# Performance work log

Hardware: AMD Instinct MI355X
Metric: run time of the kernel (lower is better)

The kernel has to match this reference:

```python
import jax, jax.numpy as jnp
import numpy as np

HIDDEN = 64
NUM_HEADS = 2
HEAD_DIM = HIDDEN // NUM_HEADS  # 32


def setup_inputs() -> dict:
    key = jax.random.key(0)
    ks = jax.random.split(key, 10)
    B, L = 8, 2048
    s = 1.0 / np.sqrt(HIDDEN)
    return {
        "hidden_states": jax.random.normal(ks[0], (B, L, HIDDEN), dtype=jnp.float32),
        "qx": jax.random.normal(ks[1], (B, L, HIDDEN), dtype=jnp.float32),
        "Wq": jax.random.uniform(ks[2], (HIDDEN, HIDDEN), jnp.float32, -s, s),
        "bq": jax.random.uniform(ks[3], (HIDDEN,), jnp.float32, -s, s),
        "Wk": jax.random.uniform(ks[4], (HIDDEN, HIDDEN), jnp.float32, -s, s),
        "bk": jax.random.uniform(ks[5], (HIDDEN,), jnp.float32, -s, s),
        "Wv": jax.random.uniform(ks[6], (HIDDEN, HIDDEN), jnp.float32, -s, s),
        "bv": jax.random.uniform(ks[7], (HIDDEN,), jnp.float32, -s, s),
        "Wo": jax.random.uniform(ks[8], (HIDDEN, HIDDEN), jnp.float32, -s, s),
        "bo": jax.random.uniform(ks[9], (HIDDEN,), jnp.float32, -s, s),
    }


def _split_heads(x):
    # [B, L, HIDDEN] -> [B, H, L, HEAD_DIM]
    B, L, _ = x.shape
    return x.reshape(B, L, NUM_HEADS, HEAD_DIM).transpose(0, 2, 1, 3)


def reference(hidden_states, qx, Wq, bq, Wk, bk, Wv, bv, Wo, bo):
    # NOTE: faithful to original - query AND value come from qx, key from hidden_states.
    q = _split_heads(qx @ Wq.T + bq)              # [B, H, Lq, D]
    k = _split_heads(hidden_states @ Wk.T + bk)   # [B, H, Lk, D]
    v = _split_heads(qx @ Wv.T + bv)              # [B, H, Lq, D]
    scores = jnp.einsum("bhqd,bhkd->bhqk", q, k) / np.sqrt(HEAD_DIM).astype(np.float32)
    probs = jax.nn.softmax(scores, axis=-1)       # [B, H, Lq, Lk]
    ctx = jnp.einsum("bhqk,bhkd->bhqd", probs, v)
    B, H, L, D = ctx.shape
    ctx = ctx.transpose(0, 2, 1, 3).reshape(B, L, H * D)
    out = ctx @ Wo.T + bo
    return out, probs
```

## Files before the change

kernel.cpp:

```cpp
#include <hip/hip_runtime.h>
#include <math.h>

#define NB 8
#define SEQ 2048
#define HID 64
#define HDIM 32
#define ROWS (NB * SEQ)
#define OUT_ELEMS (ROWS * HID)
#define QSCALE 0.25503486f

typedef __attribute__((ext_vector_type(8))) short bf16x8;
typedef __attribute__((ext_vector_type(4))) float f32x4;
typedef __attribute__((ext_vector_type(4))) uint u32x4;

__device__ __forceinline__ ushort f2bf(float f) {
    uint u = __builtin_bit_cast(uint, f);
    u += 0x7FFFu + ((u >> 16) & 1u);
    return (ushort)(u >> 16);
}
__device__ __forceinline__ float bf2f(ushort h) {
    uint u = ((uint)h) << 16;
    return __builtin_bit_cast(float, u);
}
__device__ __forceinline__ uint cvt_pk_bf16(float lo, float hi) {
    uint r;
    asm("v_cvt_pk_bf16_f32 %0, %1, %2" : "=v"(r) : "v"(lo), "v"(hi));
    return r;
}

__global__ __launch_bounds__(256, 1)
void qkv_proj_kernel(const float* __restrict__ hs, const float* __restrict__ qx,
                     const float* __restrict__ Wq, const float* __restrict__ bq,
                     const float* __restrict__ Wk, const float* __restrict__ bk,
                     const float* __restrict__ Wv, const float* __restrict__ bv,
                     ushort* __restrict__ q_hi, ushort* __restrict__ q_lo,
                     ushort* __restrict__ k_hi, ushort* __restrict__ vt_hi)
{
    __shared__ __align__(16) float xq_lds[64][64];
    __shared__ __align__(16) float xh_lds[64][64];
    __shared__ float vbuf[64][65];

    const int t  = threadIdx.x;
    const int r0 = blockIdx.x * 64;
    const int b  = r0 >> 11;

#pragma unroll
    for (int u = 0; u < 4; ++u) {
        const int idx = t + 256 * u;
        const int rr = idx >> 4, kk = (idx & 15) * 4;
        *(float4*)&xq_lds[rr][kk] = *(const float4*)(qx + (size_t)(r0 + rr) * HID + kk);
        *(float4*)&xh_lds[rr][kk] = *(const float4*)(hs + (size_t)(r0 + rr) * HID + kk);
    }
    __syncthreads();

    const int c = t & 63, w = t >> 6;
    const int rw = w * 16;
    const int h = c >> 5, d = c & 31;
    const size_t obase = ((size_t)((b * 2 + h) * SEQ) + (r0 & 2047) + rw) * 32 + d;

    {
        float4 wr[16];
#pragma unroll
        for (int i = 0; i < 16; ++i) wr[i] = *(const float4*)(Wq + c * 64 + 4 * i);
        const float bc = bq[c];
        f32x4 acc[16];
#pragma unroll
        for (int r = 0; r < 16; ++r) acc[r] = (f32x4){0.f, 0.f, 0.f, 0.f};
#pragma unroll
        for (int k4 = 0; k4 < 16; ++k4) {
#pragma unroll
            for (int r = 0; r < 16; ++r) {
                const float4 x4 = *(const float4*)&xq_lds[rw + r][k4 * 4];
                acc[r][0] += x4.x * wr[k4].x; acc[r][1] += x4.y * wr[k4].y;
                acc[r][2] += x4.z * wr[k4].z; acc[r][3] += x4.w * wr[k4].w;
            }
        }
#pragma unroll
        for (int r = 0; r < 16; ++r) {
            const float v = (acc[r][0] + acc[r][1] + acc[r][2] + acc[r][3] + bc) * QSCALE;
            const ushort hv = f2bf(v);
            q_hi[obase + (size_t)r * 32] = hv;
            q_lo[obase + (size_t)r * 32] = f2bf(v - bf2f(hv));
        }
    }
    {
        float4 wr[16];
#pragma unroll
        for (int i = 0; i < 16; ++i) wr[i] = *(const float4*)(Wk + c * 64 + 4 * i);
        const float bc = bk[c];
        f32x4 acc[16];
#pragma unroll
        for (int r = 0; r < 16; ++r) acc[r] = (f32x4){0.f, 0.f, 0.f, 0.f};
#pragma unroll
        for (int k4 = 0; k4 < 16; ++k4) {
#pragma unroll
            for (int r = 0; r < 16; ++r) {
                const float4 x4 = *(const float4*)&xh_lds[rw + r][k4 * 4];
                acc[r][0] += x4.x * wr[k4].x; acc[r][1] += x4.y * wr[k4].y;
                acc[r][2] += x4.z * wr[k4].z; acc[r][3] += x4.w * wr[k4].w;
            }
        }
#pragma unroll
        for (int r = 0; r < 16; ++r) {
            const float v = acc[r][0] + acc[r][1] + acc[r][2] + acc[r][3] + bc;
            k_hi[obase + (size_t)r * 32] = f2bf(v);
        }
    }
    {
        float4 wr[16];
#pragma unroll
        for (int i = 0; i < 16; ++i) wr[i] = *(const float4*)(Wv + c * 64 + 4 * i);
        const float bc = bv[c];
        f32x4 acc[16];
#pragma unroll
        for (int r = 0; r < 16; ++r) acc[r] = (f32x4){0.f, 0.f, 0.f, 0.f};
#pragma unroll
        for (int k4 = 0; k4 < 16; ++k4) {
#pragma unroll
            for (int r = 0; r < 16; ++r) {
                const float4 x4 = *(const float4*)&xq_lds[rw + r][k4 * 4];
                acc[r][0] += x4.x * wr[k4].x; acc[r][1] += x4.y * wr[k4].y;
                acc[r][2] += x4.z * wr[k4].z; acc[r][3] += x4.w * wr[k4].w;
            }
        }
#pragma unroll
        for (int r = 0; r < 16; ++r)
            vbuf[rw + r][c] = acc[r][0] + acc[r][1] + acc[r][2] + acc[r][3] + bc;
    }
    __syncthreads();

#pragma unroll
    for (int g = 0; g < 2; ++g) {
        const int row8 = (g * 4 + w) * 8;
        bf16x8 hi8;
#pragma unroll
        for (int e = 0; e < 8; ++e) hi8[e] = (short)f2bf(vbuf[row8 + e][c]);
        const size_t vo = ((size_t)((b * 2 + h) * 32) + d) * SEQ + (r0 & 2047) + row8;
        *reinterpret_cast<bf16x8*>(vt_hi + vo) = hi8;
    }
}

__global__ __launch_bounds__(256, 4)
void attn_kernel(const ushort* __restrict__ q_hi, const ushort* __restrict__ q_lo,
                 const ushort* __restrict__ k_hi, const ushort* __restrict__ vt_hi,
                 float* __restrict__ d_out)
{
    __shared__ float z_buf[4][32];
    __shared__ __align__(16) float ctx_buf[4][32][32];
    __shared__ __align__(16) float pstage[4][512];

    const int bid   = blockIdx.x;
    const int swz   = (bid & 7) * 128 + (bid >> 3);
    const int slice = swz >> 6;
    const int qb    = swz & 63;
    const int bb = slice >> 1, hh = slice & 1;
    const int q0 = qb * 32;

    const int tid  = threadIdx.x;
    const int w    = tid >> 6, lane = tid & 63;
    const int lg   = lane >> 4, li = lane & 15;
    const int cq0  = w * 512;

    bf16x8 aqh[2], aql[2];
#pragma unroll
    for (int rt = 0; rt < 2; ++rt) {
        const size_t qoff = ((size_t)slice * SEQ + q0 + rt * 16 + li) * 32 + lg * 8;
        aqh[rt] = *reinterpret_cast<const bf16x8*>(q_hi + qoff);
        aql[rt] = *reinterpret_cast<const bf16x8*>(q_lo + qoff);
    }

    const size_t kbase = (size_t)slice * SEQ * 32;
    const size_t vbase = (size_t)slice * 32 * SEQ;

    auto Kfrag = [&](int j16) {
        return *reinterpret_cast<const bf16x8*>(
            k_hi + kbase + (size_t)(cq0 + j16 * 16 + li) * 32 + lg * 8);
    };
    auto Vfrag = [&](int c2, int dt) {
        return *reinterpret_cast<const bf16x8*>(
            vt_hi + vbase + (size_t)(dt * 16 + li) * SEQ + cq0 + c2 * 32 + lg * 8);
    };

    float zacc[8];
#pragma unroll
    for (int i = 0; i < 8; ++i) zacc[i] = 0.f;
    {
        bf16x8 bh = Kfrag(0);
#pragma unroll 2
        for (int ct = 0; ct < 32; ++ct) {
            const bf16x8 bn = Kfrag(ct < 31 ? ct + 1 : 31);
#pragma unroll
            for (int rt = 0; rt < 2; ++rt) {
                f32x4 acc = {0.f, 0.f, 0.f, 0.f};
                acc = __builtin_amdgcn_mfma_f32_16x16x32_bf16(aqh[rt], bh, acc, 0, 0, 0);
                acc = __builtin_amdgcn_mfma_f32_16x16x32_bf16(aql[rt], bh, acc, 0, 0, 0);
#pragma unroll
                for (int r = 0; r < 4; ++r)
                    zacc[rt * 4 + r] += __builtin_amdgcn_exp2f(acc[r]);
            }
            bh = bn;
        }
    }
#pragma unroll
    for (int m = 1; m < 16; m <<= 1) {
#pragma unroll
        for (int i = 0; i < 8; ++i) zacc[i] += __shfl_xor(zacc[i], m, 64);
    }
    if (li == 0) {
#pragma unroll
        for (int rt = 0; rt < 2; ++rt)
#pragma unroll
            for (int r = 0; r < 4; ++r)
                z_buf[w][rt * 16 + lg * 4 + r] = zacc[rt * 4 + r];
    }
    __syncthreads();
    float rcpz[8];
#pragma unroll
    for (int rt = 0; rt < 2; ++rt)
#pragma unroll
        for (int r = 0; r < 4; ++r) {
            const int row = rt * 16 + lg * 4 + r;
            rcpz[rt * 4 + r] = 1.0f / (z_buf[0][row] + z_buf[1][row] +
                                       z_buf[2][row] + z_buf[3][row]);
        }

    f32x4 pacc[2][2];
#pragma unroll
    for (int rt = 0; rt < 2; ++rt)
#pragma unroll
        for (int dt = 0; dt < 2; ++dt) pacc[rt][dt] = (f32x4){0.f, 0.f, 0.f, 0.f};

    float* probs = d_out + OUT_ELEMS + ((size_t)slice * SEQ + q0) * SEQ;
    float* ps = &pstage[w][0];

    bf16x8 k0 = Kfrag(0), k1 = Kfrag(1);
    bf16x8 v0 = Vfrag(0, 0), v1 = Vfrag(0, 1);

#pragma unroll 1
    for (int c2 = 0; c2 < 16; ++c2) {
        const int cn = (c2 < 15) ? c2 + 1 : 15;
        const bf16x8 k0n = Kfrag(2 * cn),     k1n = Kfrag(2 * cn + 1);
        const bf16x8 v0n = Vfrag(cn, 0),      v1n = Vfrag(cn, 1);

        bf16x8 ap[2];
#pragma unroll
        for (int rt = 0; rt < 2; ++rt) {
            f32x4 a0 = {0.f, 0.f, 0.f, 0.f}, a1 = {0.f, 0.f, 0.f, 0.f};
            a0 = __builtin_amdgcn_mfma_f32_16x16x32_bf16(aqh[rt], k0, a0, 0, 0, 0);
            a0 = __builtin_amdgcn_mfma_f32_16x16x32_bf16(aql[rt], k0, a0, 0, 0, 0);
            a1 = __builtin_amdgcn_mfma_f32_16x16x32_bf16(aqh[rt], k1, a1, 0, 0, 0);
            a1 = __builtin_amdgcn_mfma_f32_16x16x32_bf16(aql[rt], k1, a1, 0, 0, 0);
#pragma unroll
            for (int r = 0; r < 4; ++r) {
                const int row = lg * 4 + r;
                const float p0 = __builtin_amdgcn_exp2f(a0[r]) * rcpz[rt * 4 + r];
                const float p1 = __builtin_amdgcn_exp2f(a1[r]) * rcpz[rt * 4 + r];
                ps[row * 32 + (li ^ (lg << 3))]        = p0;
                ps[row * 32 + ((16 + li) ^ (lg << 3))] = p1;
            }
#pragma unroll
            for (int u = 0; u < 2; ++u) {
                const int fid = lane + 64 * u;
                const int row = fid >> 3, c4 = fid & 7;
                const int pcb = (c4 * 4) ^ (((row >> 2) & 3) << 3);
                const f32x4 pv = *reinterpret_cast<const f32x4*>(&ps[row * 32 + pcb]);
                __builtin_nontemporal_store(pv, reinterpret_cast<f32x4*>(
                    probs + (size_t)(rt * 16 + row) * SEQ + cq0 + c2 * 32 + c4 * 4));
            }
            const int abase = li * 32 + ((lg ^ ((li >> 2) & 3)) << 3);
            const f32x4 pa = *reinterpret_cast<const f32x4*>(&ps[abase]);
            const f32x4 pb = *reinterpret_cast<const f32x4*>(&ps[abase + 4]);
            u32x4 pk;
            pk[0] = cvt_pk_bf16(pa[0], pa[1]); pk[1] = cvt_pk_bf16(pa[2], pa[3]);
            pk[2] = cvt_pk_bf16(pb[0], pb[1]); pk[3] = cvt_pk_bf16(pb[2], pb[3]);
            ap[rt] = __builtin_bit_cast(bf16x8, pk);
        }
#pragma unroll
        for (int rt = 0; rt < 2; ++rt) {
            pacc[rt][0] = __builtin_amdgcn_mfma_f32_16x16x32_bf16(ap[rt], v0, pacc[rt][0], 0, 0, 0);
            pacc[rt][1] = __builtin_amdgcn_mfma_f32_16x16x32_bf16(ap[rt], v1, pacc[rt][1], 0, 0, 0);
        }
        k0 = k0n; k1 = k1n; v0 = v0n; v1 = v1n;
    }

#pragma unroll
    for (int rt = 0; rt < 2; ++rt)
#pragma unroll
        for (int dt = 0; dt < 2; ++dt)
#pragma unroll
            for (int r = 0; r < 4; ++r)
                ctx_buf[w][rt * 16 + lg * 4 + r][dt * 16 + li] = pacc[rt][dt][r];
    __syncthreads();
    {
        const int row = tid >> 3, dq = tid & 7;
        float4 s = *reinterpret_cast<const float4*>(&ctx_buf[0][row][dq * 4]);
#pragma unroll
        for (int ww = 1; ww < 4; ++ww) {
            const float4 c = *reinterpret_cast<const float4*>(&ctx_buf[ww][row][dq * 4]);
            s.x += c.x; s.y += c.y; s.z += c.z; s.w += c.w;
        }
        *reinterpret_cast<float4*>(
            d_out + ((size_t)bb * SEQ + q0 + row) * HID + hh * HDIM + dq * 4) = s;
    }
}

__global__ __launch_bounds__(256, 1)
void out_proj_kernel(const float* __restrict__ Wo, const float* __restrict__ bo,
                     float* __restrict__ out)
{
    const int c    = threadIdx.x & 63;
    const int rloc = threadIdx.x >> 6;

    float4 wo[16];
#pragma unroll
    for (int i = 0; i < 16; ++i) wo[i] = *(const float4*)(Wo + c * 64 + 4 * i);
    const float boc = bo[c];

    for (int rg = blockIdx.x; rg < ROWS / 4; rg += gridDim.x) {
        const int row = rg * 4 + rloc;
        const float* x = out + (size_t)row * HID;
        float a = 0.f;
#pragma unroll
        for (int i = 0; i < 16; ++i) {
            const float4 x4 = *(const float4*)(x + 4 * i);
            a += x4.x * wo[i].x + x4.y * wo[i].y + x4.z * wo[i].z + x4.w * wo[i].w;
        }
        out[(size_t)row * HID + c] = a + boc;
    }
}

extern "C" void kernel_launch(void* const* d_in, const int* in_sizes, int n_in,
                              void* d_out, int out_size, void* d_ws, size_t ws_size,
                              hipStream_t stream)
{
    const float* hs = (const float*)d_in[0];
    const float* qx = (const float*)d_in[1];
    const float* Wq = (const float*)d_in[2];
    const float* bq = (const float*)d_in[3];
    const float* Wk = (const float*)d_in[4];
    const float* bk = (const float*)d_in[5];
    const float* Wv = (const float*)d_in[6];
    const float* bv = (const float*)d_in[7];
    const float* Wo = (const float*)d_in[8];
    const float* bo = (const float*)d_in[9];
    float* out = (float*)d_out;

    const size_t N = (size_t)16 * SEQ * 32;
    ushort* q_hi  = (ushort*)d_ws;
    ushort* q_lo  = q_hi + N;
    ushort* k_hi  = q_lo + N;
    ushort* vt_hi = k_hi + N;

    qkv_proj_kernel<<<256, 256, 0, stream>>>(hs, qx, Wq, bq, Wk, bk, Wv, bv,
                                             q_hi, q_lo, k_hi, vt_hi);
    attn_kernel<<<1024, 256, 0, stream>>>(q_hi, q_lo, k_hi, vt_hi, out);
    out_proj_kernel<<<512, 256, 0, stream>>>(Wo, bo, out);
}
```

Before: 105.9 us.

## Halve per-block query tile and quadruple projection grid for more parallelism

The attention kernel now handles 16 query rows per block instead of 32, which doubles the grid to 2048 blocks and raises the launch-bounds occupancy hint to 6. The QKV projection shrinks its tile from 64 to 16 rows per block and runs 1024 blocks; the output projection grid goes to 2048 blocks. The aim is better CU occupancy and latency hiding on a GPU with many CUs. In exchange, each K/V fragment loaded is reused across fewer query rows, so global/L2 traffic for K and V roughly doubles.

```diff
diff --git a/kernel.cpp b/kernel.cpp
--- a/kernel.cpp
+++ b/kernel.cpp
@@ -28,7 +28,7 @@
     return r;
 }
 
-__global__ __launch_bounds__(256, 1)
+__global__ __launch_bounds__(256, 4)
 void qkv_proj_kernel(const float* __restrict__ hs, const float* __restrict__ qx,
                      const float* __restrict__ Wq, const float* __restrict__ bq,
                      const float* __restrict__ Wk, const float* __restrict__ bk,
@@ -36,25 +36,23 @@
                      ushort* __restrict__ q_hi, ushort* __restrict__ q_lo,
                      ushort* __restrict__ k_hi, ushort* __restrict__ vt_hi)
 {
-    __shared__ __align__(16) float xq_lds[64][64];
-    __shared__ __align__(16) float xh_lds[64][64];
-    __shared__ float vbuf[64][65];
+    __shared__ __align__(16) float xq_lds[16][64];
+    __shared__ __align__(16) float xh_lds[16][64];
+    __shared__ float vbuf[16][65];
 
     const int t  = threadIdx.x;
-    const int r0 = blockIdx.x * 64;
+    const int r0 = blockIdx.x * 16;
     const int b  = r0 >> 11;
 
-#pragma unroll
-    for (int u = 0; u < 4; ++u) {
-        const int idx = t + 256 * u;
-        const int rr = idx >> 4, kk = (idx & 15) * 4;
+    {
+        const int rr = t >> 4, kk = (t & 15) * 4;
         *(float4*)&xq_lds[rr][kk] = *(const float4*)(qx + (size_t)(r0 + rr) * HID + kk);
         *(float4*)&xh_lds[rr][kk] = *(const float4*)(hs + (size_t)(r0 + rr) * HID + kk);
     }
     __syncthreads();
 
     const int c = t & 63, w = t >> 6;
-    const int rw = w * 16;
+    const int rw = w * 4;
     const int h = c >> 5, d = c & 31;
     const size_t obase = ((size_t)((b * 2 + h) * SEQ) + (r0 & 2047) + rw) * 32 + d;
 
@@ -63,20 +61,20 @@
 #pragma unroll
         for (int i = 0; i < 16; ++i) wr[i] = *(const float4*)(Wq + c * 64 + 4 * i);
         const float bc = bq[c];
-        f32x4 acc[16];
-#pragma unroll
-        for (int r = 0; r < 16; ++r) acc[r] = (f32x4){0.f, 0.f, 0.f, 0.f};
+        f32x4 acc[4];
+#pragma unroll
+        for (int r = 0; r < 4; ++r) acc[r] = (f32x4){0.f, 0.f, 0.f, 0.f};
 #pragma unroll
         for (int k4 = 0; k4 < 16; ++k4) {
 #pragma unroll
-            for (int r = 0; r < 16; ++r) {
+            for (int r = 0; r < 4; ++r) {
                 const float4 x4 = *(const float4*)&xq_lds[rw + r][k4 * 4];
                 acc[r][0] += x4.x * wr[k4].x; acc[r][1] += x4.y * wr[k4].y;
                 acc[r][2] += x4.z * wr[k4].z; acc[r][3] += x4.w * wr[k4].w;
             }
         }
 #pragma unroll
-        for (int r = 0; r < 16; ++r) {
+        for (int r = 0; r < 4; ++r) {
             const float v = (acc[r][0] + acc[r][1] + acc[r][2] + acc[r][3] + bc) * QSCALE;
             const ushort hv = f2bf(v);
             q_hi[obase + (size_t)r * 32] = hv;
@@ -88,20 +86,20 @@
 #pragma unroll
         for (int i = 0; i < 16; ++i) wr[i] = *(const float4*)(Wk + c * 64 + 4 * i);
         const float bc = bk[c];
-        f32x4 acc[16];
-#pragma unroll
-        for (int r = 0; r < 16; ++r) acc[r] = (f32x4){0.f, 0.f, 0.f, 0.f};
+        f32x4 acc[4];
+#pragma unroll
+        for (int r = 0; r < 4; ++r) acc[r] = (f32x4){0.f, 0.f, 0.f, 0.f};
 #pragma unroll
         for (int k4 = 0; k4 < 16; ++k4) {
 #pragma unroll
-            for (int r = 0; r < 16; ++r) {
+            for (int r = 0; r < 4; ++r) {
                 const float4 x4 = *(const float4*)&xh_lds[rw + r][k4 * 4];
                 acc[r][0] += x4.x * wr[k4].x; acc[r][1] += x4.y * wr[k4].y;
                 acc[r][2] += x4.z * wr[k4].z; acc[r][3] += x4.w * wr[k4].w;
             }
         }
 #pragma unroll
-        for (int r = 0; r < 16; ++r) {
+        for (int r = 0; r < 4; ++r) {
             const float v = acc[r][0] + acc[r][1] + acc[r][2] + acc[r][3] + bc;
             k_hi[obase + (size_t)r * 32] = f2bf(v);
         }
@@ -111,63 +109,59 @@
 #pragma unroll
         for (int i = 0; i < 16; ++i) wr[i] = *(const float4*)(Wv + c * 64 + 4 * i);
         const float bc = bv[c];
-        f32x4 acc[16];
-#pragma unroll
-        for (int r = 0; r < 16; ++r) acc[r] = (f32x4){0.f, 0.f, 0.f, 0.f};
+        f32x4 acc[4];
+#pragma unroll
+        for (int r = 0; r < 4; ++r) acc[r] = (f32x4){0.f, 0.f, 0.f, 0.f};
 #pragma unroll
         for (int k4 = 0; k4 < 16; ++k4) {
 #pragma unroll
-            for (int r = 0; r < 16; ++r) {
+            for (int r = 0; r < 4; ++r) {
                 const float4 x4 = *(const float4*)&xq_lds[rw + r][k4 * 4];
                 acc[r][0] += x4.x * wr[k4].x; acc[r][1] += x4.y * wr[k4].y;
                 acc[r][2] += x4.z * wr[k4].z; acc[r][3] += x4.w * wr[k4].w;
             }
         }
 #pragma unroll
-        for (int r = 0; r < 16; ++r)
+        for (int r = 0; r < 4; ++r)
             vbuf[rw + r][c] = acc[r][0] + acc[r][1] + acc[r][2] + acc[r][3] + bc;
     }
     __syncthreads();
 
-#pragma unroll
-    for (int g = 0; g < 2; ++g) {
-        const int row8 = (g * 4 + w) * 8;
+    if (t < 128) {
+        const int cc = t & 63, half = t >> 6;
+        const int h2 = cc >> 5, d2 = cc & 31;
         bf16x8 hi8;
 #pragma unroll
-        for (int e = 0; e < 8; ++e) hi8[e] = (short)f2bf(vbuf[row8 + e][c]);
-        const size_t vo = ((size_t)((b * 2 + h) * 32) + d) * SEQ + (r0 & 2047) + row8;
+        for (int e = 0; e < 8; ++e) hi8[e] = (short)f2bf(vbuf[half * 8 + e][cc]);
+        const size_t vo = ((size_t)((b * 2 + h2) * 32) + d2) * SEQ + (r0 & 2047) + half * 8;
         *reinterpret_cast<bf16x8*>(vt_hi + vo) = hi8;
     }
 }
 
-__global__ __launch_bounds__(256, 4)
+__global__ __launch_bounds__(256, 6)
 void attn_kernel(const ushort* __restrict__ q_hi, const ushort* __restrict__ q_lo,
                  const ushort* __restrict__ k_hi, const ushort* __restrict__ vt_hi,
                  float* __restrict__ d_out)
 {
-    __shared__ float z_buf[4][32];
-    __shared__ __align__(16) float ctx_buf[4][32][32];
+    __shared__ float z_buf[4][16];
+    __shared__ __align__(16) float ctx_buf[4][16][32];
     __shared__ __align__(16) float pstage[4][512];
 
     const int bid   = blockIdx.x;
-    const int swz   = (bid & 7) * 128 + (bid >> 3);
-    const int slice = swz >> 6;
-    const int qb    = swz & 63;
+    const int swz   = (bid & 7) * 256 + (bid >> 3);
+    const int slice = swz >> 7;
+    const int qb    = swz & 127;
     const int bb = slice >> 1, hh = slice & 1;
-    const int q0 = qb * 32;
+    const int q0 = qb * 16;
 
     const int tid  = threadIdx.x;
     const int w    = tid >> 6, lane = tid & 63;
     const int lg   = lane >> 4, li = lane & 15;
     const int cq0  = w * 512;
 
-    bf16x8 aqh[2], aql[2];
-#pragma unroll
-    for (int rt = 0; rt < 2; ++rt) {
-        const size_t qoff = ((size_t)slice * SEQ + q0 + rt * 16 + li) * 32 + lg * 8;
-        aqh[rt] = *reinterpret_cast<const bf16x8*>(q_hi + qoff);
-        aql[rt] = *reinterpret_cast<const bf16x8*>(q_lo + qoff);
-    }
+    const size_t qoff = ((size_t)slice * SEQ + q0 + li) * 32 + lg * 8;
+    const bf16x8 aqh = *reinterpret_cast<const bf16x8*>(q_hi + qoff);
+    const bf16x8 aql = *reinterpret_cast<const bf16x8*>(q_lo + qoff);
 
     const size_t kbase = (size_t)slice * SEQ * 32;
     const size_t vbase = (size_t)slice * 32 * SEQ;
@@ -181,54 +175,38 @@
             vt_hi + vbase + (size_t)(dt * 16 + li) * SEQ + cq0 + c2 * 32 + lg * 8);
     };
 
-    float zacc[8];
-#pragma unroll
-    for (int i = 0; i < 8; ++i) zacc[i] = 0.f;
+    float zacc[4] = {0.f, 0.f, 0.f, 0.f};
     {
         bf16x8 bh = Kfrag(0);
 #pragma unroll 2
         for (int ct = 0; ct < 32; ++ct) {
             const bf16x8 bn = Kfrag(ct < 31 ? ct + 1 : 31);
-#pragma unroll
-            for (int rt = 0; rt < 2; ++rt) {
-                f32x4 acc = {0.f, 0.f, 0.f, 0.f};
-                acc = __builtin_amdgcn_mfma_f32_16x16x32_bf16(aqh[rt], bh, acc, 0, 0, 0);
-                acc = __builtin_amdgcn_mfma_f32_16x16x32_bf16(aql[rt], bh, acc, 0, 0, 0);
-#pragma unroll
-                for (int r = 0; r < 4; ++r)
-                    zacc[rt * 4 + r] += __builtin_amdgcn_exp2f(acc[r]);
-            }
+            f32x4 acc = {0.f, 0.f, 0.f, 0.f};
+            acc = __builtin_amdgcn_mfma_f32_16x16x32_bf16(aqh, bh, acc, 0, 0, 0);
+            acc = __builtin_amdgcn_mfma_f32_16x16x32_bf16(aql, bh, acc, 0, 0, 0);
+#pragma unroll
+            for (int r = 0; r < 4; ++r) zacc[r] += __builtin_amdgcn_exp2f(acc[r]);
             bh = bn;
         }
     }
 #pragma unroll
     for (int m = 1; m < 16; m <<= 1) {
 #pragma unroll
-        for (int i = 0; i < 8; ++i) zacc[i] += __shfl_xor(zacc[i], m, 64);
+        for (int r = 0; r < 4; ++r) zacc[r] += __shfl_xor(zacc[r], m, 64);
     }
     if (li == 0) {
 #pragma unroll
-        for (int rt = 0; rt < 2; ++rt)
-#pragma unroll
-            for (int r = 0; r < 4; ++r)
-                z_buf[w][rt * 16 + lg * 4 + r] = zacc[rt * 4 + r];
+        for (int r = 0; r < 4; ++r) z_buf[w][lg * 4 + r] = zacc[r];
     }
     __syncthreads();
-    float rcpz[8];
-#pragma unroll
-    for (int rt = 0; rt < 2; ++rt)
-#pragma unroll
-        for (int r = 0; r < 4; ++r) {
-            const int row = rt * 16 + lg * 4 + r;
-            rcpz[rt * 4 + r] = 1.0f / (z_buf[0][row] + z_buf[1][row] +
-                                       z_buf[2][row] + z_buf[3][row]);
-        }
-
-    f32x4 pacc[2][2];
-#pragma unroll
-    for (int rt = 0; rt < 2; ++rt)
-#pragma unroll
-        for (int dt = 0; dt < 2; ++dt) pacc[rt][dt] = (f32x4){0.f, 0.f, 0.f, 0.f};
+    float rcpz[4];
+#pragma unroll
+    for (int r = 0; r < 4; ++r) {
+        const int row = lg * 4 + r;
+        rcpz[r] = 1.0f / (z_buf[0][row] + z_buf[1][row] + z_buf[2][row] + z_buf[3][row]);
+    }
+
+    f32x4 pacc[2] = {{0.f,0.f,0.f,0.f}, {0.f,0.f,0.f,0.f}};
 
     float* probs = d_out + OUT_ELEMS + ((size_t)slice * SEQ + q0) * SEQ;
     float* ps = &pstage[w][0];
@@ -242,56 +220,48 @@
         const bf16x8 k0n = Kfrag(2 * cn),     k1n = Kfrag(2 * cn + 1);
         const bf16x8 v0n = Vfrag(cn, 0),      v1n = Vfrag(cn, 1);
 
-        bf16x8 ap[2];
-#pragma unroll
-        for (int rt = 0; rt < 2; ++rt) {
-            f32x4 a0 = {0.f, 0.f, 0.f, 0.f}, a1 = {0.f, 0.f, 0.f, 0.f};
-            a0 = __builtin_amdgcn_mfma_f32_16x16x32_bf16(aqh[rt], k0, a0, 0, 0, 0);
-            a0 = __builtin_amdgcn_mfma_f32_16x16x32_bf16(aql[rt], k0, a0, 0, 0, 0);
-            a1 = __builtin_amdgcn_mfma_f32_16x16x32_bf16(aqh[rt], k1, a1, 0, 0, 0);
-            a1 = __builtin_amdgcn_mfma_f32_16x16x32_bf16(aql[rt], k1, a1, 0, 0, 0);
-#pragma unroll
-            for (int r = 0; r < 4; ++r) {
-                const int row = lg * 4 + r;
-                const float p0 = __builtin_amdgcn_exp2f(a0[r]) * rcpz[rt * 4 + r];
-                const float p1 = __builtin_amdgcn_exp2f(a1[r]) * rcpz[rt * 4 + r];
-                ps[row * 32 + (li ^ (lg << 3))]        = p0;
-                ps[row * 32 + ((16 + li) ^ (lg << 3))] = p1;
-            }
-#pragma unroll
-            for (int u = 0; u < 2; ++u) {
-                const int fid = lane + 64 * u;
-                const int row = fid >> 3, c4 = fid & 7;
-                const int pcb = (c4 * 4) ^ (((row >> 2) & 3) << 3);
-                const f32x4 pv = *reinterpret_cast<const f32x4*>(&ps[row * 32 + pcb]);
-                __builtin_nontemporal_store(pv, reinterpret_cast<f32x4*>(
-                    probs + (size_t)(rt * 16 + row) * SEQ + cq0 + c2 * 32 + c4 * 4));
-            }
-            const int abase = li * 32 + ((lg ^ ((li >> 2) & 3)) << 3);
-            const f32x4 pa = *reinterpret_cast<const f32x4*>(&ps[abase]);
-            const f32x4 pb = *reinterpret_cast<const f32x4*>(&ps[abase + 4]);
-            u32x4 pk;
-            pk[0] = cvt_pk_bf16(pa[0], pa[1]); pk[1] = cvt_pk_bf16(pa[2], pa[3]);
-            pk[2] = cvt_pk_bf16(pb[0], pb[1]); pk[3] = cvt_pk_bf16(pb[2], pb[3]);
-            ap[rt] = __builtin_bit_cast(bf16x8, pk);
-        }
-#pragma unroll
-        for (int rt = 0; rt < 2; ++rt) {
-            pacc[rt][0] = __builtin_amdgcn_mfma_f32_16x16x32_bf16(ap[rt], v0, pacc[rt][0], 0, 0, 0);
-            pacc[rt][1] = __builtin_amdgcn_mfma_f32_16x16x32_bf16(ap[rt], v1, pacc[rt][1], 0, 0, 0);
-        }
+        f32x4 a0 = {0.f, 0.f, 0.f, 0.f}, a1 = {0.f, 0.f, 0.f, 0.f};
+        a0 = __builtin_amdgcn_mfma_f32_16x16x32_bf16(aqh, k0, a0, 0, 0, 0);
+        a0 = __builtin_amdgcn_mfma_f32_16x16x32_bf16(aql, k0, a0, 0, 0, 0);
+        a1 = __builtin_amdgcn_mfma_f32_16x16x32_bf16(aqh, k1, a1, 0, 0, 0);
+        a1 = __builtin_amdgcn_mfma_f32_16x16x32_bf16(aql, k1, a1, 0, 0, 0);
+#pragma unroll
+        for (int r = 0; r < 4; ++r) {
+            const int row = lg * 4 + r;
+            const float p0 = __builtin_amdgcn_exp2f(a0[r]) * rcpz[r];
+            const float p1 = __builtin_amdgcn_exp2f(a1[r]) * rcpz[r];
+            ps[row * 32 + (li ^ (lg << 3))]        = p0;
+            ps[row * 32 + ((16 + li) ^ (lg << 3))] = p1;
+        }
+#pragma unroll
+        for (int u = 0; u < 2; ++u) {
+            const int fid = lane + 64 * u;
+            const int row = fid >> 3, c4 = fid & 7;
+            const int pcb = (c4 * 4) ^ (((row >> 2) & 3) << 3);
+            const f32x4 pv = *reinterpret_cast<const f32x4*>(&ps[row * 32 + pcb]);
+            __builtin_nontemporal_store(pv, reinterpret_cast<f32x4*>(
+                probs + (size_t)row * SEQ + cq0 + c2 * 32 + c4 * 4));
+        }
+        const int abase = li * 32 + ((lg ^ ((li >> 2) & 3)) << 3);
+        const f32x4 pa = *reinterpret_cast<const f32x4*>(&ps[abase]);
+        const f32x4 pb = *reinterpret_cast<const f32x4*>(&ps[abase + 4]);
+        u32x4 pk;
+        pk[0] = cvt_pk_bf16(pa[0], pa[1]); pk[1] = cvt_pk_bf16(pa[2], pa[3]);
+        pk[2] = cvt_pk_bf16(pb[0], pb[1]); pk[3] = cvt_pk_bf16(pb[2], pb[3]);
+        const bf16x8 ap = __builtin_bit_cast(bf16x8, pk);
+        pacc[0] = __builtin_amdgcn_mfma_f32_16x16x32_bf16(ap, v0, pacc[0], 0, 0, 0);
+        pacc[1] = __builtin_amdgcn_mfma_f32_16x16x32_bf16(ap, v1, pacc[1], 0, 0, 0);
+
         k0 = k0n; k1 = k1n; v0 = v0n; v1 = v1n;
     }
 
 #pragma unroll
-    for (int rt = 0; rt < 2; ++rt)
-#pragma unroll
-        for (int dt = 0; dt < 2; ++dt)
-#pragma unroll
-            for (int r = 0; r < 4; ++r)
-                ctx_buf[w][rt * 16 + lg * 4 + r][dt * 16 + li] = pacc[rt][dt][r];
+    for (int dt = 0; dt < 2; ++dt)
+#pragma unroll
+        for (int r = 0; r < 4; ++r)
+            ctx_buf[w][lg * 4 + r][dt * 16 + li] = pacc[dt][r];
     __syncthreads();
-    {
+    if (tid < 128) {
         const int row = tid >> 3, dq = tid & 7;
         float4 s = *reinterpret_cast<const float4*>(&ctx_buf[0][row][dq * 4]);
 #pragma unroll
@@ -304,7 +274,7 @@
     }
 }
 
-__global__ __launch_bounds__(256, 1)
+__global__ __launch_bounds__(256, 4)
 void out_proj_kernel(const float* __restrict__ Wo, const float* __restrict__ bo,
                      float* __restrict__ out)
 {
@@ -351,8 +321,8 @@
     ushort* k_hi  = q_lo + N;
     ushort* vt_hi = k_hi + N;
 
-    qkv_proj_kernel<<<256, 256, 0, stream>>>(hs, qx, Wq, bq, Wk, bk, Wv, bv,
-                                             q_hi, q_lo, k_hi, vt_hi);
-    attn_kernel<<<1024, 256, 0, stream>>>(q_hi, q_lo, k_hi, vt_hi, out);
-    out_proj_kernel<<<512, 256, 0, stream>>>(Wo, bo, out);
-}
+    qkv_proj_kernel<<<1024, 256, 0, stream>>>(hs, qx, Wq, bq, Wk, bk, Wv, bv,
+                                              q_hi, q_lo, k_hi, vt_hi);
+    attn_kernel<<<2048, 256, 0, stream>>>(q_hi, q_lo, k_hi, vt_hi, out);
+    out_proj_kernel<<<2048, 256, 0, stream>>>(Wo, bo, out);
+}
```

New measurement: 132.4 us. 25.0% more time.

## Split softmax denominator into separate kernel and pipeline K/V through LDS ring

Applied to the files above, without the earlier changes.

The row-sum pass moves into its own zsum kernel, which handles 64 query rows per block and writes reciprocal denominators to workspace. The attention kernel now uses 512 threads per 64-row query block. It stages K and V tiles into a triple-buffered LDS ring with global_load_lds and explicit vmcnt waits, and splits the work across waves by row tile and column half, so no cross-wave context reduction is needed. Probabilities are written as full 64-column rows through a shared padded buffer, aiming for better coalescing and K/V reuse, at the cost of an extra launch and more barriers per tile.

```diff
diff --git a/kernel.cpp b/kernel.cpp
--- a/kernel.cpp
+++ b/kernel.cpp
@@ -27,6 +27,11 @@
     asm("v_cvt_pk_bf16_f32 %0, %1, %2" : "=v"(r) : "v"(lo), "v"(hi));
     return r;
 }
+__device__ __forceinline__ void glds16(const ushort* g, ushort* l) {
+    __builtin_amdgcn_global_load_lds(
+        (const __attribute__((address_space(1))) uint*)(g),
+        (__attribute__((address_space(3))) uint*)(l), 16, 0, 0);
+}
 
 __global__ __launch_bounds__(256, 1)
 void qkv_proj_kernel(const float* __restrict__ hs, const float* __restrict__ qx,
@@ -67,14 +72,13 @@
 #pragma unroll
         for (int r = 0; r < 16; ++r) acc[r] = (f32x4){0.f, 0.f, 0.f, 0.f};
 #pragma unroll
-        for (int k4 = 0; k4 < 16; ++k4) {
+        for (int k4 = 0; k4 < 16; ++k4)
 #pragma unroll
             for (int r = 0; r < 16; ++r) {
                 const float4 x4 = *(const float4*)&xq_lds[rw + r][k4 * 4];
                 acc[r][0] += x4.x * wr[k4].x; acc[r][1] += x4.y * wr[k4].y;
                 acc[r][2] += x4.z * wr[k4].z; acc[r][3] += x4.w * wr[k4].w;
             }
-        }
 #pragma unroll
         for (int r = 0; r < 16; ++r) {
             const float v = (acc[r][0] + acc[r][1] + acc[r][2] + acc[r][3] + bc) * QSCALE;
@@ -92,14 +96,13 @@
 #pragma unroll
         for (int r = 0; r < 16; ++r) acc[r] = (f32x4){0.f, 0.f, 0.f, 0.f};
 #pragma unroll
-        for (int k4 = 0; k4 < 16; ++k4) {
+        for (int k4 = 0; k4 < 16; ++k4)
 #pragma unroll
             for (int r = 0; r < 16; ++r) {
                 const float4 x4 = *(const float4*)&xh_lds[rw + r][k4 * 4];
                 acc[r][0] += x4.x * wr[k4].x; acc[r][1] += x4.y * wr[k4].y;
                 acc[r][2] += x4.z * wr[k4].z; acc[r][3] += x4.w * wr[k4].w;
             }
-        }
 #pragma unroll
         for (int r = 0; r < 16; ++r) {
             const float v = acc[r][0] + acc[r][1] + acc[r][2] + acc[r][3] + bc;
@@ -115,14 +118,13 @@
 #pragma unroll
         for (int r = 0; r < 16; ++r) acc[r] = (f32x4){0.f, 0.f, 0.f, 0.f};
 #pragma unroll
-        for (int k4 = 0; k4 < 16; ++k4) {
+        for (int k4 = 0; k4 < 16; ++k4)
 #pragma unroll
             for (int r = 0; r < 16; ++r) {
                 const float4 x4 = *(const float4*)&xq_lds[rw + r][k4 * 4];
                 acc[r][0] += x4.x * wr[k4].x; acc[r][1] += x4.y * wr[k4].y;
                 acc[r][2] += x4.z * wr[k4].z; acc[r][3] += x4.w * wr[k4].w;
             }
-        }
 #pragma unroll
         for (int r = 0; r < 16; ++r)
             vbuf[rw + r][c] = acc[r][0] + acc[r][1] + acc[r][2] + acc[r][3] + bc;
@@ -140,168 +142,187 @@
     }
 }
 
-__global__ __launch_bounds__(256, 4)
-void attn_kernel(const ushort* __restrict__ q_hi, const ushort* __restrict__ q_lo,
-                 const ushort* __restrict__ k_hi, const ushort* __restrict__ vt_hi,
-                 float* __restrict__ d_out)
-{
-    __shared__ float z_buf[4][32];
-    __shared__ __align__(16) float ctx_buf[4][32][32];
-    __shared__ __align__(16) float pstage[4][512];
+__global__ __launch_bounds__(256, 2)
+void zsum_kernel(const ushort* __restrict__ q_hi, const ushort* __restrict__ q_lo,
+                 const ushort* __restrict__ k_hi, float* __restrict__ rz_ws)
+{
+    __shared__ float z_buf[4][64];
 
     const int bid   = blockIdx.x;
-    const int swz   = (bid & 7) * 128 + (bid >> 3);
-    const int slice = swz >> 6;
-    const int qb    = swz & 63;
-    const int bb = slice >> 1, hh = slice & 1;
-    const int q0 = qb * 32;
+    const int swz   = (bid & 7) * 64 + (bid >> 3);
+    const int slice = swz >> 5;
+    const int qb    = swz & 31;
+    const int q0 = qb * 64;
 
     const int tid  = threadIdx.x;
     const int w    = tid >> 6, lane = tid & 63;
     const int lg   = lane >> 4, li = lane & 15;
     const int cq0  = w * 512;
 
-    bf16x8 aqh[2], aql[2];
-#pragma unroll
-    for (int rt = 0; rt < 2; ++rt) {
+    bf16x8 aqh[4], aql[4];
+#pragma unroll
+    for (int rt = 0; rt < 4; ++rt) {
         const size_t qoff = ((size_t)slice * SEQ + q0 + rt * 16 + li) * 32 + lg * 8;
-        aqh[rt] = *reinterpret_cast<const bf16x8*>(q_hi + qoff);
-        aql[rt] = *reinterpret_cast<const bf16x8*>(q_lo + qoff);
-    }
-
+        aqh[rt] = *(const bf16x8*)(q_hi + qoff);
+        aql[rt] = *(const bf16x8*)(q_lo + qoff);
+    }
     const size_t kbase = (size_t)slice * SEQ * 32;
-    const size_t vbase = (size_t)slice * 32 * SEQ;
-
-    auto Kfrag = [&](int j16) {
-        return *reinterpret_cast<const bf16x8*>(
-            k_hi + kbase + (size_t)(cq0 + j16 * 16 + li) * 32 + lg * 8);
+    auto Kf = [&](int j16) {
+        return *(const bf16x8*)(k_hi + kbase + (size_t)(cq0 + j16 * 16 + li) * 32 + lg * 8);
     };
-    auto Vfrag = [&](int c2, int dt) {
-        return *reinterpret_cast<const bf16x8*>(
-            vt_hi + vbase + (size_t)(dt * 16 + li) * SEQ + cq0 + c2 * 32 + lg * 8);
-    };
-
-    float zacc[8];
-#pragma unroll
-    for (int i = 0; i < 8; ++i) zacc[i] = 0.f;
-    {
-        bf16x8 bh = Kfrag(0);
+
+    float zacc[16];
+#pragma unroll
+    for (int i = 0; i < 16; ++i) zacc[i] = 0.f;
+    bf16x8 bh = Kf(0);
 #pragma unroll 2
-        for (int ct = 0; ct < 32; ++ct) {
-            const bf16x8 bn = Kfrag(ct < 31 ? ct + 1 : 31);
-#pragma unroll
-            for (int rt = 0; rt < 2; ++rt) {
-                f32x4 acc = {0.f, 0.f, 0.f, 0.f};
-                acc = __builtin_amdgcn_mfma_f32_16x16x32_bf16(aqh[rt], bh, acc, 0, 0, 0);
-                acc = __builtin_amdgcn_mfma_f32_16x16x32_bf16(aql[rt], bh, acc, 0, 0, 0);
-#pragma unroll
-                for (int r = 0; r < 4; ++r)
-                    zacc[rt * 4 + r] += __builtin_amdgcn_exp2f(acc[r]);
-            }
-            bh = bn;
-        }
-    }
-#pragma unroll
-    for (int m = 1; m < 16; m <<= 1) {
-#pragma unroll
-        for (int i = 0; i < 8; ++i) zacc[i] += __shfl_xor(zacc[i], m, 64);
-    }
+    for (int ct = 0; ct < 32; ++ct) {
+        const bf16x8 bn = Kf(ct < 31 ? ct + 1 : 31);
+#pragma unroll
+        for (int rt = 0; rt < 4; ++rt) {
+            f32x4 a = {0.f, 0.f, 0.f, 0.f};
+            a = __builtin_amdgcn_mfma_f32_16x16x32_bf16(aqh[rt], bh, a, 0, 0, 0);
+            a = __builtin_amdgcn_mfma_f32_16x16x32_bf16(aql[rt], bh, a, 0, 0, 0);
+#pragma unroll
+            for (int r = 0; r < 4; ++r) zacc[rt * 4 + r] += __builtin_amdgcn_exp2f(a[r]);
+        }
+        bh = bn;
+    }
+#pragma unroll
+    for (int m = 1; m < 16; m <<= 1)
+#pragma unroll
+        for (int i = 0; i < 16; ++i) zacc[i] += __shfl_xor(zacc[i], m, 64);
     if (li == 0) {
 #pragma unroll
-        for (int rt = 0; rt < 2; ++rt)
+        for (int rt = 0; rt < 4; ++rt)
 #pragma unroll
             for (int r = 0; r < 4; ++r)
                 z_buf[w][rt * 16 + lg * 4 + r] = zacc[rt * 4 + r];
     }
     __syncthreads();
-    float rcpz[8];
-#pragma unroll
-    for (int rt = 0; rt < 2; ++rt)
-#pragma unroll
-        for (int r = 0; r < 4; ++r) {
-            const int row = rt * 16 + lg * 4 + r;
-            rcpz[rt * 4 + r] = 1.0f / (z_buf[0][row] + z_buf[1][row] +
-                                       z_buf[2][row] + z_buf[3][row]);
-        }
-
-    f32x4 pacc[2][2];
-#pragma unroll
-    for (int rt = 0; rt < 2; ++rt)
-#pragma unroll
-        for (int dt = 0; dt < 2; ++dt) pacc[rt][dt] = (f32x4){0.f, 0.f, 0.f, 0.f};
-
+    if (tid < 64) {
+        const float z = z_buf[0][tid] + z_buf[1][tid] + z_buf[2][tid] + z_buf[3][tid];
+        rz_ws[(size_t)slice * SEQ + q0 + tid] = 1.0f / z;
+    }
+}
+
+__global__ __launch_bounds__(512, 4)
+void attn_kernel(const ushort* __restrict__ q_hi, const ushort* __restrict__ q_lo,
+                 const ushort* __restrict__ k_hi, const ushort* __restrict__ vt_hi,
+                 const float* __restrict__ rz_ws, float* __restrict__ d_out)
+{
+    __shared__ __align__(16) ushort kbuf[3][2048];
+    __shared__ __align__(16) ushort vbuf[3][2048];
+    __shared__ __align__(16) float  ps[64 * 68];
+
+    const int bid   = blockIdx.x;
+    const int swz   = (bid & 7) * 64 + (bid >> 3);
+    const int slice = swz >> 5;
+    const int qb    = swz & 31;
+    const int bb = slice >> 1, hh = slice & 1;
+    const int q0 = qb * 64;
+
+    const int tid  = threadIdx.x;
+    const int wid  = tid >> 6, lane = tid & 63;
+    const int lg   = lane >> 4, li = lane & 15;
+    const int rt   = wid & 3;
+    const int cs   = wid >> 2;
+
+    const size_t qoff = ((size_t)slice * SEQ + q0 + rt * 16 + li) * 32 + lg * 8;
+    const bf16x8 aqh = *(const bf16x8*)(q_hi + qoff);
+    const bf16x8 aql = *(const bf16x8*)(q_lo + qoff);
+
+    float rcpz[4];
+#pragma unroll
+    for (int r = 0; r < 4; ++r)
+        rcpz[r] = rz_ws[(size_t)slice * SEQ + q0 + rt * 16 + lg * 4 + r];
+
+    const ushort* kslice = k_hi + (size_t)slice * SEQ * 32;
+    const ushort* vslice = vt_hi + (size_t)slice * 32 * SEQ;
     float* probs = d_out + OUT_ELEMS + ((size_t)slice * SEQ + q0) * SEQ;
-    float* ps = &pstage[w][0];
-
-    bf16x8 k0 = Kfrag(0), k1 = Kfrag(1);
-    bf16x8 v0 = Vfrag(0, 0), v1 = Vfrag(0, 1);
+
+    auto STAGE = [&](int t, int ring) {
+        const int j0 = t * 64;
+        if (wid < 4) {
+            const int col = wid * 16 + (lane >> 2);
+            const int cg  = (lane & 3) ^ ((lane >> 2) & 3);
+            glds16(kslice + (size_t)(j0 + col) * 32 + cg * 8,
+                   &kbuf[ring][wid * 512 + lane * 8]);
+        } else {
+            const int w2  = wid - 4;
+            const int row = w2 * 8 + (lane >> 3);
+            const int cg  = (lane & 7) ^ (row & 7);
+            glds16(vslice + (size_t)row * SEQ + j0 + cg * 8,
+                   &vbuf[ring][w2 * 512 + lane * 8]);
+        }
+    };
+
+    STAGE(0, 0); STAGE(1, 1);
+
+    f32x4 pacc = {0.f, 0.f, 0.f, 0.f};
+    int rc = 0, rs = 2;
 
 #pragma unroll 1
-    for (int c2 = 0; c2 < 16; ++c2) {
-        const int cn = (c2 < 15) ? c2 + 1 : 15;
-        const bf16x8 k0n = Kfrag(2 * cn),     k1n = Kfrag(2 * cn + 1);
-        const bf16x8 v0n = Vfrag(cn, 0),      v1n = Vfrag(cn, 1);
-
-        bf16x8 ap[2];
-#pragma unroll
-        for (int rt = 0; rt < 2; ++rt) {
-            f32x4 a0 = {0.f, 0.f, 0.f, 0.f}, a1 = {0.f, 0.f, 0.f, 0.f};
-            a0 = __builtin_amdgcn_mfma_f32_16x16x32_bf16(aqh[rt], k0, a0, 0, 0, 0);
-            a0 = __builtin_amdgcn_mfma_f32_16x16x32_bf16(aql[rt], k0, a0, 0, 0, 0);
-            a1 = __builtin_amdgcn_mfma_f32_16x16x32_bf16(aqh[rt], k1, a1, 0, 0, 0);
-            a1 = __builtin_amdgcn_mfma_f32_16x16x32_bf16(aql[rt], k1, a1, 0, 0, 0);
-#pragma unroll
-            for (int r = 0; r < 4; ++r) {
-                const int row = lg * 4 + r;
-                const float p0 = __builtin_amdgcn_exp2f(a0[r]) * rcpz[rt * 4 + r];
-                const float p1 = __builtin_amdgcn_exp2f(a1[r]) * rcpz[rt * 4 + r];
-                ps[row * 32 + (li ^ (lg << 3))]        = p0;
-                ps[row * 32 + ((16 + li) ^ (lg << 3))] = p1;
-            }
-#pragma unroll
-            for (int u = 0; u < 2; ++u) {
-                const int fid = lane + 64 * u;
-                const int row = fid >> 3, c4 = fid & 7;
-                const int pcb = (c4 * 4) ^ (((row >> 2) & 3) << 3);
-                const f32x4 pv = *reinterpret_cast<const f32x4*>(&ps[row * 32 + pcb]);
-                __builtin_nontemporal_store(pv, reinterpret_cast<f32x4*>(
-                    probs + (size_t)(rt * 16 + row) * SEQ + cq0 + c2 * 32 + c4 * 4));
-            }
-            const int abase = li * 32 + ((lg ^ ((li >> 2) & 3)) << 3);
-            const f32x4 pa = *reinterpret_cast<const f32x4*>(&ps[abase]);
-            const f32x4 pb = *reinterpret_cast<const f32x4*>(&ps[abase + 4]);
+    for (int t = 0; t < 32; ++t) {
+        asm volatile("s_waitcnt lgkmcnt(0)" ::: "memory");
+        __builtin_amdgcn_s_barrier();
+        __builtin_amdgcn_sched_barrier(0);
+        if (t + 2 < 32) STAGE(t + 2, rs);
+        if (t == 0)       asm volatile("s_waitcnt vmcnt(2)" ::: "memory");
+        else if (t == 1)  asm volatile("s_waitcnt vmcnt(4)" ::: "memory");
+        else if (t <= 29) asm volatile("s_waitcnt vmcnt(6)" ::: "memory");
+        else if (t == 30) asm volatile("s_waitcnt vmcnt(5)" ::: "memory");
+        else              asm volatile("s_waitcnt vmcnt(4)" ::: "memory");
+        __builtin_amdgcn_s_barrier();
+        __builtin_amdgcn_sched_barrier(0);
+
+#pragma unroll
+        for (int h2 = 0; h2 < 2; ++h2) {
+            const int c16 = cs * 2 + h2;
+            const bf16x8 bk = *(const bf16x8*)
+                &kbuf[rc][(c16 * 16 + li) * 32 + ((lg ^ (li & 3)) * 8)];
+            f32x4 a = {0.f, 0.f, 0.f, 0.f};
+            a = __builtin_amdgcn_mfma_f32_16x16x32_bf16(aqh, bk, a, 0, 0, 0);
+            a = __builtin_amdgcn_mfma_f32_16x16x32_bf16(aql, bk, a, 0, 0, 0);
+#pragma unroll
+            for (int r = 0; r < 4; ++r)
+                ps[(rt * 16 + lg * 4 + r) * 68 + c16 * 16 + li] =
+                    __builtin_amdgcn_exp2f(a[r]) * rcpz[r];
+        }
+        asm volatile("s_waitcnt lgkmcnt(0)" ::: "memory");
+        __builtin_amdgcn_s_barrier();
+        __builtin_amdgcn_sched_barrier(0);
+
+#pragma unroll
+        for (int ch = 0; ch < 2; ++ch) {
+            const int pbase = (rt * 16 + li) * 68 + ch * 32 + lg * 8;
+            const f32x4 pa = *(const f32x4*)&ps[pbase];
+            const f32x4 pb = *(const f32x4*)&ps[pbase + 4];
             u32x4 pk;
             pk[0] = cvt_pk_bf16(pa[0], pa[1]); pk[1] = cvt_pk_bf16(pa[2], pa[3]);
             pk[2] = cvt_pk_bf16(pb[0], pb[1]); pk[3] = cvt_pk_bf16(pb[2], pb[3]);
-            ap[rt] = __builtin_bit_cast(bf16x8, pk);
-        }
-#pragma unroll
-        for (int rt = 0; rt < 2; ++rt) {
-            pacc[rt][0] = __builtin_amdgcn_mfma_f32_16x16x32_bf16(ap[rt], v0, pacc[rt][0], 0, 0, 0);
-            pacc[rt][1] = __builtin_amdgcn_mfma_f32_16x16x32_bf16(ap[rt], v1, pacc[rt][1], 0, 0, 0);
-        }
-        k0 = k0n; k1 = k1n; v0 = v0n; v1 = v1n;
-    }
-
-#pragma unroll
-    for (int rt = 0; rt < 2; ++rt)
-#pragma unroll
-        for (int dt = 0; dt < 2; ++dt)
-#pragma unroll
-            for (int r = 0; r < 4; ++r)
-                ctx_buf[w][rt * 16 + lg * 4 + r][dt * 16 + li] = pacc[rt][dt][r];
-    __syncthreads();
-    {
-        const int row = tid >> 3, dq = tid & 7;
-        float4 s = *reinterpret_cast<const float4*>(&ctx_buf[0][row][dq * 4]);
-#pragma unroll
-        for (int ww = 1; ww < 4; ++ww) {
-            const float4 c = *reinterpret_cast<const float4*>(&ctx_buf[ww][row][dq * 4]);
-            s.x += c.x; s.y += c.y; s.z += c.z; s.w += c.w;
-        }
-        *reinterpret_cast<float4*>(
-            d_out + ((size_t)bb * SEQ + q0 + row) * HID + hh * HDIM + dq * 4) = s;
-    }
+            const bf16x8 ap = __builtin_bit_cast(bf16x8, pk);
+            const int vr = cs * 16 + li;
+            const bf16x8 bv = *(const bf16x8*)
+                &vbuf[rc][vr * 64 + (((ch * 4 + lg) ^ (vr & 7)) * 8)];
+            pacc = __builtin_amdgcn_mfma_f32_16x16x32_bf16(ap, bv, pacc, 0, 0, 0);
+        }
+#pragma unroll
+        for (int u = 0; u < 2; ++u) {
+            const int fid = tid + 512 * u;
+            const int row = fid >> 4, c4 = fid & 15;
+            const f32x4 pv = *(const f32x4*)&ps[row * 68 + c4 * 4];
+            *(f32x4*)(probs + (size_t)row * SEQ + t * 64 + c4 * 4) = pv;
+        }
+
+        rc = (rc == 2) ? 0 : rc + 1;
+        rs = (rs == 2) ? 0 : rs + 1;
+    }
+
+#pragma unroll
+    for (int r = 0; r < 4; ++r)
+        d_out[((size_t)bb * SEQ + q0 + rt * 16 + lg * 4 + r) * HID
+              + hh * HDIM + cs * 16 + li] = pacc[r];
 }
 
 __global__ __launch_bounds__(256, 1)
@@ -350,9 +371,11 @@
     ushort* q_lo  = q_hi + N;
     ushort* k_hi  = q_lo + N;
     ushort* vt_hi = k_hi + N;
+    float*  rz_ws = (float*)(vt_hi + N);
 
     qkv_proj_kernel<<<256, 256, 0, stream>>>(hs, qx, Wq, bq, Wk, bk, Wv, bv,
                                              q_hi, q_lo, k_hi, vt_hi);
-    attn_kernel<<<1024, 256, 0, stream>>>(q_hi, q_lo, k_hi, vt_hi, out);
+    zsum_kernel<<<512, 256, 0, stream>>>(q_hi, q_lo, k_hi, rz_ws);
+    attn_kernel<<<512, 512, 0, stream>>>(q_hi, q_lo, k_hi, vt_hi, rz_ws, out);
     out_proj_kernel<<<512, 256, 0, stream>>>(Wo, bo, out);
 }
```

After: 104.6 us (median of 4 runs). Within noise of the previous version (-1.2%).
